# Optimization experiments

Hardware: AMD Instinct MI355X
Metric: run time of the kernel (lower is better)

The kernel has to match this reference:

```python
import jax, jax.numpy as jnp
import numpy as np

HEAD_SIZE = 64
HEADS = 12

def _rope(x):
    # x: [B, L, d]; bert4torch interleaved RoPE: q*cos + rotate_every_two(q)*sin
    L, d = x.shape[-2], x.shape[-1]
    inv_freq = 1.0 / (10000.0 ** (jnp.arange(0, d, 2, dtype=jnp.float32) / d))
    ang = jnp.arange(L, dtype=jnp.float32)[:, None] * inv_freq  # [L, d/2]
    sin = jnp.repeat(jnp.sin(ang), 2, axis=-1)  # [L, d]
    cos = jnp.repeat(jnp.cos(ang), 2, axis=-1)  # [L, d]
    x2 = jnp.stack([-x[..., 1::2], x[..., ::2]], axis=-1).reshape(x.shape)
    return x * cos + x2 * sin

def setup_inputs() -> dict:
    key = jax.random.key(0)
    ks = jax.random.split(key, 4)
    B, L, H = 2, 2048, 1024
    inputs = jax.random.normal(ks[0], (B, L, H), dtype=jnp.float32)
    mask = jnp.ones((B, L), dtype=jnp.int32)
    Wp = jax.random.normal(ks[1], (H, 2 * HEAD_SIZE), dtype=jnp.float32) * (1.0 / np.sqrt(H))
    bp = jnp.zeros((2 * HEAD_SIZE,), dtype=jnp.float32)
    Wq = jax.random.normal(ks[2], (2 * HEAD_SIZE, 2 * HEADS), dtype=jnp.float32) * (1.0 / np.sqrt(2 * HEAD_SIZE))
    bq = jnp.zeros((2 * HEADS,), dtype=jnp.float32)
    return {"inputs": inputs, "mask": mask, "Wp": Wp, "bp": bp, "Wq": Wq, "bq": bq}

def reference(inputs, mask, Wp, bp, Wq, bq):
    B, L, _ = inputs.shape
    seq_out = inputs @ Wp + bp                          # [B, L, 2*hs]
    qw, kw = seq_out[..., :HEAD_SIZE], seq_out[..., HEAD_SIZE:]
    qw, kw = _rope(qw), _rope(kw)
    scores = jnp.einsum('bmd,bnd->bmn', qw, kw) / jnp.sqrt(jnp.float32(HEAD_SIZE))  # [B, L, L]
    # chunk(heads, -1) + stack(-2) == reshape(B, L, heads, 2); transpose(1,2) -> [B, H, L, 2]
    bias = (seq_out @ Wq + bq).reshape(B, L, HEADS, 2) / 2.0
    bias = jnp.transpose(bias, (0, 2, 1, 3))            # [B, H, L, 2]
    logits = scores[:, None] + bias[..., :1] + jnp.swapaxes(bias[..., 1:], 2, 3)  # [B, H, L, L]
    m = mask.astype(bool)
    neg_inf = jnp.float32(-jnp.inf)
    logits = jnp.where(m[:, None, :, None], logits, neg_inf)
    logits = jnp.where(m[:, None, None, :], logits, neg_inf)
    tril = jnp.tril(jnp.ones((L, L), dtype=logits.dtype), -1)
    logits = logits - tril * jnp.float32(1e12)
    return logits
```

## Files before the change

### kernel.cpp

```cpp
#include <hip/hip_runtime.h>
#include <math.h>

#define LSEQ 2048
#define NB 2
#define HDIM 1024
#define NKV 128
#define MALL (NB*LSEQ)
#define KSPLIT 4

__global__ __launch_bounds__(256) void k1_gemm(const float* __restrict__ A,
                                               const float* __restrict__ Wp,
                                               float* __restrict__ Cp) {
    const int nt    = blockIdx.x & 1;
    const int split = blockIdx.x >> 1;
    const int m0 = blockIdx.y * 64;
    const int n0 = nt * 64;
    __shared__ float As[32][68];
    __shared__ float Bs[32][64];
    const int tid = threadIdx.x;
    const int tm = tid & 15;
    const int tn = tid >> 4;
    float acc[4][4] = {};
    for (int kc = 0; kc < 8; ++kc) {
        const int k0 = split*256 + kc*32;
        #pragma unroll
        for (int p = 0; p < 2; ++p) {
            int idx = tid + 256*p;
            int row = idx >> 3, kq = idx & 7;
            float4 a = *(const float4*)(A + (size_t)(m0+row)*HDIM + k0 + 4*kq);
            As[4*kq+0][row] = a.x;
            As[4*kq+1][row] = a.y;
            As[4*kq+2][row] = a.z;
            As[4*kq+3][row] = a.w;
        }
        #pragma unroll
        for (int p = 0; p < 2; ++p) {
            int idx = tid + 256*p;
            int r = idx >> 4, c = idx & 15;
            *(float4*)(&Bs[r][4*c]) = *(const float4*)(Wp + (size_t)(k0+r)*NKV + n0 + 4*c);
        }
        __syncthreads();
        #pragma unroll
        for (int kk = 0; kk < 32; ++kk) {
            float4 av = *(const float4*)(&As[kk][4*tm]);
            float4 bv = *(const float4*)(&Bs[kk][4*tn]);
            float aa[4] = {av.x, av.y, av.z, av.w};
            float bb[4] = {bv.x, bv.y, bv.z, bv.w};
            #pragma unroll
            for (int i = 0; i < 4; ++i)
                #pragma unroll
                for (int j = 0; j < 4; ++j)
                    acc[i][j] = fmaf(aa[i], bb[j], acc[i][j]);
        }
        __syncthreads();
    }
    float* outp = Cp + (size_t)split*MALL*NKV;
    #pragma unroll
    for (int i = 0; i < 4; ++i) {
        float4 v = make_float4(acc[i][0], acc[i][1], acc[i][2], acc[i][3]);
        *(float4*)(outp + (size_t)(m0 + 4*tm + i)*NKV + n0 + 4*tn) = v;
    }
}

__global__ __launch_bounds__(64) void k2_rope_bias(const float* __restrict__ Cp,
        const float* __restrict__ bp, const float* __restrict__ Wq,
        const float* __restrict__ bq, float* __restrict__ qwout,
        float* __restrict__ kwout, float* __restrict__ biasQ,
        float* __restrict__ biasK) {
    const int row = blockIdx.x;
    const int b = row >> 11;
    const int l = row & (LSEQ - 1);
    const int t = threadIdx.x;
    float x0 = bp[2*t], x1 = bp[2*t+1];
    #pragma unroll
    for (int s = 0; s < KSPLIT; ++s) {
        const float* r = Cp + (size_t)s*MALL*NKV + (size_t)row*NKV;
        x0 += r[2*t];
        x1 += r[2*t+1];
    }
    const int p = t & 31;
    float inv = exp2f(-0.41524101186098287f * (float)p);
    float ang = (float)l * inv;
    float sn = sinf(ang), cs = cosf(ang);
    float y0 = x0*cs - x1*sn;
    float y1 = x1*cs + x0*sn;
    float* dst = (t < 32) ? (qwout + (size_t)row*64) : (kwout + (size_t)row*64);
    dst[2*p]   = y0;
    dst[2*p+1] = y1;
    float res = 0.f;
    for (int j = 0; j < 24; ++j) {
        float part = fmaf(x0, Wq[(2*t)*24 + j], x1 * Wq[(2*t+1)*24 + j]);
        #pragma unroll
        for (int off = 32; off > 0; off >>= 1)
            part += __shfl_xor(part, off);
        if (t == j) res = part;
    }
    if (t < 24) {
        float v = (res + bq[t]) * 0.5f;
        int h = t >> 1;
        float* bb = (t & 1) ? biasK : biasQ;
        bb[((size_t)b*12 + h)*LSEQ + l] = v;
    }
}

__global__ __launch_bounds__(256, 2) void k3_scores(const float* __restrict__ qw,
        const float* __restrict__ kwv, const float* __restrict__ biasQ,
        const float* __restrict__ biasK, const int* __restrict__ mask,
        float* __restrict__ out) {
    const int m0 = blockIdx.x * 4;
    const int b  = blockIdx.y;
    const int tid = threadIdx.x;
    const int nl = tid & 127;
    const int g  = tid >> 7;
    __shared__ float kws[128 * 68];

    const size_t rowbase = (size_t)b * LSEQ;
    const int mA = m0 + 2*g, mB = mA + 1;

    float4 q0[16], q1[16];
    {
        const float4* qp0 = (const float4*)(qw + (rowbase + mA)*64);
        const float4* qp1 = (const float4*)(qw + (rowbase + mB)*64);
        #pragma unroll
        for (int j = 0; j < 16; ++j) { q0[j] = qp0[j]; q1[j] = qp1[j]; }
    }
    float bq0[12], bq1[12];
    #pragma unroll
    for (int h = 0; h < 12; ++h) {
        const float* bqp = biasQ + ((size_t)b*12 + h)*LSEQ;
        bq0[h] = bqp[mA];
        bq1[h] = bqp[mB];
    }
    const bool okmA = mask[rowbase + mA] != 0;
    const bool okmB = mask[rowbase + mB] != 0;
    const size_t outbase = (size_t)b * 12 * LSEQ * LSEQ;

    for (int c = 0; c < 16; ++c) {
        const int nbase = c * 128;
        __syncthreads();
        #pragma unroll
        for (int p = 0; p < 8; ++p) {
            int f4 = tid + 256*p;
            int r = f4 >> 4, q16 = f4 & 15;
            float4 v = *(const float4*)(kwv + (rowbase + nbase + r)*64 + 4*q16);
            *(float4*)(&kws[r*68 + 4*q16]) = v;
        }
        __syncthreads();

        const int n = nbase + nl;
        float acc0 = 0.f, acc1 = 0.f;
        const float4* kr = (const float4*)(&kws[nl * 68]);
        #pragma unroll
        for (int j = 0; j < 16; ++j) {
            float4 kv = kr[j];
            acc0 = fmaf(q0[j].x, kv.x, acc0);
            acc0 = fmaf(q0[j].y, kv.y, acc0);
            acc0 = fmaf(q0[j].z, kv.z, acc0);
            acc0 = fmaf(q0[j].w, kv.w, acc0);
            acc1 = fmaf(q1[j].x, kv.x, acc1);
            acc1 = fmaf(q1[j].y, kv.y, acc1);
            acc1 = fmaf(q1[j].z, kv.z, acc1);
            acc1 = fmaf(q1[j].w, kv.w, acc1);
        }
        acc0 *= 0.125f;
        acc1 *= 0.125f;

        const bool okn = mask[rowbase + n] != 0;
        const float penA = (mA > n) ? 1e12f : 0.f;
        const float penB = (mB > n) ? 1e12f : 0.f;
        const bool okA = okmA && okn;
        const bool okB = okmB && okn;
        size_t offA = outbase + (size_t)mA * LSEQ + n;
        const float* bkp = biasK + (size_t)b*12*LSEQ + n;
        #pragma unroll
        for (int h = 0; h < 12; ++h) {
            float bk = bkp[(size_t)h * LSEQ];
            float v0 = acc0 + bq0[h] + bk;
            v0 = okA ? v0 : -INFINITY;
            v0 -= penA;
            float v1 = acc1 + bq1[h] + bk;
            v1 = okB ? v1 : -INFINITY;
            v1 -= penB;
            __builtin_nontemporal_store(v0, &out[offA + (size_t)h*LSEQ*LSEQ]);
            __builtin_nontemporal_store(v1, &out[offA + LSEQ + (size_t)h*LSEQ*LSEQ]);
        }
    }
}

extern "C" void kernel_launch(void* const* d_in, const int* in_sizes, int n_in,
                              void* d_out, int out_size, void* d_ws, size_t ws_size,
                              hipStream_t stream) {
    const float* inputs = (const float*)d_in[0];
    const int*   mask   = (const int*)  d_in[1];
    const float* Wp     = (const float*)d_in[2];
    const float* bp     = (const float*)d_in[3];
    const float* Wq     = (const float*)d_in[4];
    const float* bq     = (const float*)d_in[5];
    float* out = (float*)d_out;

    float* Cp  = (float*)d_ws;
    float* qwb = Cp  + (size_t)KSPLIT*MALL*NKV;
    float* kwb = qwb + (size_t)MALL*64;
    float* bQ  = kwb + (size_t)MALL*64;
    float* bK  = bQ  + (size_t)NB*12*LSEQ;

    k1_gemm     <<<dim3(8, 64),   256, 0, stream>>>(inputs, Wp, Cp);
    k2_rope_bias<<<dim3(MALL),     64, 0, stream>>>(Cp, bp, Wq, bq, qwb, kwb, bQ, bK);
    k3_scores   <<<dim3(512, 2), 256, 0, stream>>>(qwb, kwb, bQ, bK, mask, out);
}
```

Baseline: 458.1 us.

## Restructure score kernel: per-wave rows, float4 stores, swizzled double-buffered K tiles

```diff
diff --git a/kernel.cpp b/kernel.cpp
--- a/kernel.cpp
+++ b/kernel.cpp
@@ -103,86 +103,105 @@
     }
 }
 
-__global__ __launch_bounds__(256, 2) void k3_scores(const float* __restrict__ qw,
+__global__ __launch_bounds__(512, 2) void k3_scores(const float* __restrict__ qw,
         const float* __restrict__ kwv, const float* __restrict__ biasQ,
         const float* __restrict__ biasK, const int* __restrict__ mask,
         float* __restrict__ out) {
-    const int m0 = blockIdx.x * 4;
-    const int b  = blockIdx.y;
+    extern __shared__ float kws[];
+    const int m0  = blockIdx.x * 8;
+    const int b   = blockIdx.y;
     const int tid = threadIdx.x;
-    const int nl = tid & 127;
-    const int g  = tid >> 7;
-    __shared__ float kws[128 * 68];
-
+    const int w   = tid >> 6;
+    const int l   = tid & 63;
     const size_t rowbase = (size_t)b * LSEQ;
-    const int mA = m0 + 2*g, mB = mA + 1;
-
-    float4 q0[16], q1[16];
+    const int m = m0 + w;
+    const int swz = l & 7;
+
+    float4 q4[16];
     {
-        const float4* qp0 = (const float4*)(qw + (rowbase + mA)*64);
-        const float4* qp1 = (const float4*)(qw + (rowbase + mB)*64);
-        #pragma unroll
-        for (int j = 0; j < 16; ++j) { q0[j] = qp0[j]; q1[j] = qp1[j]; }
-    }
-    float bq0[12], bq1[12];
-    #pragma unroll
-    for (int h = 0; h < 12; ++h) {
-        const float* bqp = biasQ + ((size_t)b*12 + h)*LSEQ;
-        bq0[h] = bqp[mA];
-        bq1[h] = bqp[mB];
-    }
-    const bool okmA = mask[rowbase + mA] != 0;
-    const bool okmB = mask[rowbase + mB] != 0;
-    const size_t outbase = (size_t)b * 12 * LSEQ * LSEQ;
-
-    for (int c = 0; c < 16; ++c) {
-        const int nbase = c * 128;
-        __syncthreads();
-        #pragma unroll
-        for (int p = 0; p < 8; ++p) {
-            int f4 = tid + 256*p;
-            int r = f4 >> 4, q16 = f4 & 15;
-            float4 v = *(const float4*)(kwv + (rowbase + nbase + r)*64 + 4*q16);
-            *(float4*)(&kws[r*68 + 4*q16]) = v;
-        }
-        __syncthreads();
-
-        const int n = nbase + nl;
-        float acc0 = 0.f, acc1 = 0.f;
-        const float4* kr = (const float4*)(&kws[nl * 68]);
+        const float4* qp = (const float4*)(qw + (rowbase + m)*64);
+        #pragma unroll
+        for (int j = 0; j < 16; ++j) q4[j] = qp[j];
+    }
+    float bqh[12];
+    #pragma unroll
+    for (int h = 0; h < 12; ++h) bqh[h] = biasQ[((size_t)b*12 + h)*LSEQ + m];
+    const bool okm = mask[rowbase + m] != 0;
+    const size_t outrow = (size_t)b*12*LSEQ*LSEQ + (size_t)m*LSEQ;
+
+    #pragma unroll
+    for (int p = 0; p < 8; ++p) {
+        int F = tid + 512*p;
+        int r = F >> 4, qd = F & 15;
+        float4 v = *(const float4*)(kwv + (rowbase + r)*64 + 4*qd);
+        *(float4*)(&kws[r*64 + 4*(qd ^ ((r>>2)&7))]) = v;
+    }
+    asm volatile("s_waitcnt lgkmcnt(0)" ::: "memory");
+    __builtin_amdgcn_s_barrier();
+    asm volatile("" ::: "memory");
+
+    for (int s = 0; s < 8; ++s) {
+        const int cur = (s & 1) * 16384;
+        const int nxt = ((s + 1) & 1) * 16384;
+        const bool more = (s + 1) < 8;
+
+        float4 pre[8];
+        if (more) {
+            const int n1 = (s + 1) * 256;
+            #pragma unroll
+            for (int p = 0; p < 8; ++p) {
+                int F = tid + 512*p;
+                int r = F >> 4, qd = F & 15;
+                pre[p] = *(const float4*)(kwv + (rowbase + n1 + r)*64 + 4*qd);
+            }
+        }
+
+        float acc0 = 0.f, acc1 = 0.f, acc2 = 0.f, acc3 = 0.f;
+        const float* kb = kws + cur + 256*l;
         #pragma unroll
         for (int j = 0; j < 16; ++j) {
-            float4 kv = kr[j];
-            acc0 = fmaf(q0[j].x, kv.x, acc0);
-            acc0 = fmaf(q0[j].y, kv.y, acc0);
-            acc0 = fmaf(q0[j].z, kv.z, acc0);
-            acc0 = fmaf(q0[j].w, kv.w, acc0);
-            acc1 = fmaf(q1[j].x, kv.x, acc1);
-            acc1 = fmaf(q1[j].y, kv.y, acc1);
-            acc1 = fmaf(q1[j].z, kv.z, acc1);
-            acc1 = fmaf(q1[j].w, kv.w, acc1);
-        }
-        acc0 *= 0.125f;
-        acc1 *= 0.125f;
-
-        const bool okn = mask[rowbase + n] != 0;
-        const float penA = (mA > n) ? 1e12f : 0.f;
-        const float penB = (mB > n) ? 1e12f : 0.f;
-        const bool okA = okmA && okn;
-        const bool okB = okmB && okn;
-        size_t offA = outbase + (size_t)mA * LSEQ + n;
-        const float* bkp = biasK + (size_t)b*12*LSEQ + n;
+            const int qo = 4*(j ^ swz);
+            float4 k0 = *(const float4*)(kb + qo);
+            float4 k1 = *(const float4*)(kb + 64 + qo);
+            float4 k2 = *(const float4*)(kb + 128 + qo);
+            float4 k3 = *(const float4*)(kb + 192 + qo);
+            float4 qv = q4[j];
+            acc0 = fmaf(qv.x,k0.x,fmaf(qv.y,k0.y,fmaf(qv.z,k0.z,fmaf(qv.w,k0.w,acc0))));
+            acc1 = fmaf(qv.x,k1.x,fmaf(qv.y,k1.y,fmaf(qv.z,k1.z,fmaf(qv.w,k1.w,acc1))));
+            acc2 = fmaf(qv.x,k2.x,fmaf(qv.y,k2.y,fmaf(qv.z,k2.z,fmaf(qv.w,k2.w,acc2))));
+            acc3 = fmaf(qv.x,k3.x,fmaf(qv.y,k3.y,fmaf(qv.z,k3.z,fmaf(qv.w,k3.w,acc3))));
+        }
+
+        const int nq = s*256 + 4*l;
+        int4 mq = *(const int4*)(mask + rowbase + nq);
+        float t0 = (okm && mq.x) ? fmaf(acc0, 0.125f, (m > nq+0) ? -1e12f : 0.f) : -INFINITY;
+        float t1 = (okm && mq.y) ? fmaf(acc1, 0.125f, (m > nq+1) ? -1e12f : 0.f) : -INFINITY;
+        float t2 = (okm && mq.z) ? fmaf(acc2, 0.125f, (m > nq+2) ? -1e12f : 0.f) : -INFINITY;
+        float t3 = (okm && mq.w) ? fmaf(acc3, 0.125f, (m > nq+3) ? -1e12f : 0.f) : -INFINITY;
+        const float* bkbase = biasK + (size_t)b*12*LSEQ + nq;
+        float* op = out + outrow + nq;
         #pragma unroll
         for (int h = 0; h < 12; ++h) {
-            float bk = bkp[(size_t)h * LSEQ];
-            float v0 = acc0 + bq0[h] + bk;
-            v0 = okA ? v0 : -INFINITY;
-            v0 -= penA;
-            float v1 = acc1 + bq1[h] + bk;
-            v1 = okB ? v1 : -INFINITY;
-            v1 -= penB;
-            __builtin_nontemporal_store(v0, &out[offA + (size_t)h*LSEQ*LSEQ]);
-            __builtin_nontemporal_store(v1, &out[offA + LSEQ + (size_t)h*LSEQ*LSEQ]);
+            float4 bk = *(const float4*)(bkbase + (size_t)h*LSEQ);
+            float bq = bqh[h];
+            float4 v;
+            v.x = t0 + bq + bk.x;
+            v.y = t1 + bq + bk.y;
+            v.z = t2 + bq + bk.z;
+            v.w = t3 + bq + bk.w;
+            *(float4*)(op + (size_t)h*LSEQ*LSEQ) = v;
+        }
+
+        if (more) {
+            #pragma unroll
+            for (int p = 0; p < 8; ++p) {
+                int F = tid + 512*p;
+                int r = F >> 4, qd = F & 15;
+                *(float4*)(&kws[nxt + r*64 + 4*(qd ^ ((r>>2)&7))]) = pre[p];
+            }
+            asm volatile("s_waitcnt lgkmcnt(0)" ::: "memory");
+            __builtin_amdgcn_s_barrier();
+            asm volatile("" ::: "memory");
         }
     }
 }
@@ -206,5 +225,5 @@
 
     k1_gemm     <<<dim3(8, 64),   256, 0, stream>>>(inputs, Wp, Cp);
     k2_rope_bias<<<dim3(MALL),     64, 0, stream>>>(Cp, bp, Wq, bq, qwb, kwb, bQ, bK);
-    k3_scores   <<<dim3(512, 2), 256, 0, stream>>>(qwb, kwb, bQ, bK, mask, out);
-}
+    k3_scores   <<<dim3(256, 2), 512, 131072, stream>>>(qwb, kwb, bQ, bK, mask, out);
+}
```

Result: slower. 521.8 us (+13.9%).

## Stage score rows in shared memory and write output with 128-bit nontemporal stores

Applied to the files above, without the earlier changes.

```diff
diff --git a/kernel.cpp b/kernel.cpp
--- a/kernel.cpp
+++ b/kernel.cpp
@@ -7,6 +7,8 @@
 #define NKV 128
 #define MALL (NB*LSEQ)
 #define KSPLIT 4
+
+typedef float vf4 __attribute__((ext_vector_type(4)));
 
 __global__ __launch_bounds__(256) void k1_gemm(const float* __restrict__ A,
                                                const float* __restrict__ Wp,
@@ -113,6 +115,8 @@
     const int nl = tid & 127;
     const int g  = tid >> 7;
     __shared__ float kws[128 * 68];
+    __shared__ float ss[4 * LSEQ];
+    __shared__ float bql[48];
 
     const size_t rowbase = (size_t)b * LSEQ;
     const int mA = m0 + 2*g, mB = mA + 1;
@@ -124,16 +128,10 @@
         #pragma unroll
         for (int j = 0; j < 16; ++j) { q0[j] = qp0[j]; q1[j] = qp1[j]; }
     }
-    float bq0[12], bq1[12];
-    #pragma unroll
-    for (int h = 0; h < 12; ++h) {
-        const float* bqp = biasQ + ((size_t)b*12 + h)*LSEQ;
-        bq0[h] = bqp[mA];
-        bq1[h] = bqp[mB];
-    }
-    const bool okmA = mask[rowbase + mA] != 0;
-    const bool okmB = mask[rowbase + mB] != 0;
-    const size_t outbase = (size_t)b * 12 * LSEQ * LSEQ;
+    if (tid < 48) {
+        int h = tid >> 2, r = tid & 3;
+        bql[tid] = biasQ[((size_t)b*12 + h)*LSEQ + m0 + r];
+    }
 
     for (int c = 0; c < 16; ++c) {
         const int nbase = c * 128;
@@ -162,27 +160,50 @@
             acc1 = fmaf(q1[j].z, kv.z, acc1);
             acc1 = fmaf(q1[j].w, kv.w, acc1);
         }
-        acc0 *= 0.125f;
-        acc1 *= 0.125f;
-
-        const bool okn = mask[rowbase + n] != 0;
-        const float penA = (mA > n) ? 1e12f : 0.f;
-        const float penB = (mB > n) ? 1e12f : 0.f;
-        const bool okA = okmA && okn;
-        const bool okB = okmB && okn;
-        size_t offA = outbase + (size_t)mA * LSEQ + n;
-        const float* bkp = biasK + (size_t)b*12*LSEQ + n;
-        #pragma unroll
-        for (int h = 0; h < 12; ++h) {
-            float bk = bkp[(size_t)h * LSEQ];
-            float v0 = acc0 + bq0[h] + bk;
-            v0 = okA ? v0 : -INFINITY;
-            v0 -= penA;
-            float v1 = acc1 + bq1[h] + bk;
-            v1 = okB ? v1 : -INFINITY;
-            v1 -= penB;
-            __builtin_nontemporal_store(v0, &out[offA + (size_t)h*LSEQ*LSEQ]);
-            __builtin_nontemporal_store(v1, &out[offA + LSEQ + (size_t)h*LSEQ*LSEQ]);
+        ss[2*g*LSEQ + n]     = acc0 * 0.125f;
+        ss[(2*g+1)*LSEQ + n] = acc1 * 0.125f;
+    }
+    __syncthreads();
+
+    bool okm[4];
+    #pragma unroll
+    for (int r = 0; r < 4; ++r) okm[r] = mask[rowbase + m0 + r] != 0;
+    const int nA = 4*tid, nB = 4*tid + 1024;
+    const int4 mqA = *(const int4*)(mask + rowbase + nA);
+    const int4 mqB = *(const int4*)(mask + rowbase + nB);
+    const float* bkb = biasK + (size_t)b*12*LSEQ;
+    float* const ob = out + ((size_t)b*12*LSEQ + (size_t)m0)*LSEQ;
+
+    #pragma unroll
+    for (int h = 0; h < 12; ++h) {
+        const float4 bkA = *(const float4*)(bkb + (size_t)h*LSEQ + nA);
+        const float4 bkB = *(const float4*)(bkb + (size_t)h*LSEQ + nB);
+        float* const oh = ob + (size_t)h*LSEQ*LSEQ;
+        #pragma unroll
+        for (int r = 0; r < 4; ++r) {
+            const float bqv = bql[h*4 + r];
+            const int m = m0 + r;
+            const bool om = okm[r];
+            {
+                float4 s = *(const float4*)(&ss[r*LSEQ + nA]);
+                vf4 v;
+                float t;
+                t = s.x + bqv + bkA.x; t = (om && mqA.x) ? t : -INFINITY; v.x = t - ((m > nA+0) ? 1e12f : 0.f);
+                t = s.y + bqv + bkA.y; t = (om && mqA.y) ? t : -INFINITY; v.y = t - ((m > nA+1) ? 1e12f : 0.f);
+                t = s.z + bqv + bkA.z; t = (om && mqA.z) ? t : -INFINITY; v.z = t - ((m > nA+2) ? 1e12f : 0.f);
+                t = s.w + bqv + bkA.w; t = (om && mqA.w) ? t : -INFINITY; v.w = t - ((m > nA+3) ? 1e12f : 0.f);
+                __builtin_nontemporal_store(v, (vf4*)(oh + (size_t)r*LSEQ + nA));
+            }
+            {
+                float4 s = *(const float4*)(&ss[r*LSEQ + nB]);
+                vf4 v;
+                float t;
+                t = s.x + bqv + bkB.x; t = (om && mqB.x) ? t : -INFINITY; v.x = t - ((m > nB+0) ? 1e12f : 0.f);
+                t = s.y + bqv + bkB.y; t = (om && mqB.y) ? t : -INFINITY; v.y = t - ((m > nB+1) ? 1e12f : 0.f);
+                t = s.z + bqv + bkB.z; t = (om && mqB.z) ? t : -INFINITY; v.z = t - ((m > nB+2) ? 1e12f : 0.f);
+                t = s.w + bqv + bkB.w; t = (om && mqB.w) ? t : -INFINITY; v.w = t - ((m > nB+3) ? 1e12f : 0.f);
+                __builtin_nontemporal_store(v, (vf4*)(oh + (size_t)r*LSEQ + nB));
+            }
         }
     }
 }
```

Measured after the change: 466.2 us. No clear change (+1.8%).
